# Optimization experiments

Hardware: AMD Instinct MI355X
Metric: run time of the kernel (lower is better)

The kernel has to match this reference:

```python
import jax, jax.numpy as jnp
import numpy as np

# pywt db4 analysis filters (dec_lo, dec_hi), length 8
DEC_LO = np.array([-0.010597401784997278, 0.032883011666982945, 0.030841381835986965,
                   -0.18703481171888114, -0.02798376941698385, 0.6308807679295904,
                   0.7148465705525415, 0.23037781330885523], dtype=np.float32)
DEC_HI = np.array([-0.23037781330885523, 0.7148465705525415, -0.6308807679295904,
                   -0.02798376941698385, 0.18703481171888114, 0.030841381835986965,
                   -0.032883011666982945, -0.010597401784997278], dtype=np.float32)


def setup_inputs() -> dict:
    key = jax.random.key(0)
    x = jax.random.normal(key, (32, 3, 512, 512), dtype=jnp.float32)
    dec = jnp.stack([jnp.asarray(DEC_LO), jnp.asarray(DEC_HI)])  # (2, 8)
    return {"x": x, "dec": dec}


def _afb1d_last(x, dec):
    """Analysis filter bank along last axis: circular pad (end), stride-2
    cross-correlation with lo/hi filters. x: (..., L) -> (lo, hi) each (..., L//2)."""
    L = x.shape[-1]
    taps = dec.shape[-1]
    pad = taps - 1
    xp = jnp.concatenate([x, x[..., :pad]], axis=-1)          # circular pad at end
    flat = xp.reshape(-1, 1, xp.shape[-1])                    # (N, 1, L+pad)
    out = jax.lax.conv_general_dilated(
        flat, dec[:, None, :], window_strides=(2,), padding='VALID',
        dimension_numbers=('NCH', 'OIH', 'NCH'))              # (N, 2, L//2)
    out = out.reshape(*x.shape[:-1], 2, L // 2)
    return out[..., 0, :], out[..., 1, :]


def reference(x, dec):
    B, C, H, W = x.shape
    xr = x.reshape(B * C, H, W)
    # row pass (along W)
    lo_w, hi_w = _afb1d_last(xr, dec)                         # (BC, H, W//2)
    # column pass (along H): move H to last axis
    lo_t = jnp.swapaxes(lo_w, -2, -1)                         # (BC, W//2, H)
    hi_t = jnp.swapaxes(hi_w, -2, -1)
    ll, lh = _afb1d_last(lo_t, dec)                           # (BC, W//2, H//2)
    hl, hh = _afb1d_last(hi_t, dec)
    coeffs = jnp.stack([ll, lh, hl, hh], axis=1)              # (BC, 4, W//2, H//2)
    coeffs = jnp.swapaxes(coeffs, -2, -1)                     # (BC, 4, H//2, W//2)
    return coeffs.reshape(B, C * 4, H // 2, W // 2)
```

## Files before the change

kernel.cpp:

```cpp
#include <hip/hip_runtime.h>


#define TI 8
#define TJ 64
#define PR (2*TI + 6)
#define PC 136
#define NG ((PR * PC) / 4)
#define HH 512
#define WW 512

typedef float v2f __attribute__((ext_vector_type(2)));
typedef const __attribute__((address_space(1))) void gas_t;
typedef __attribute__((address_space(3))) void las_t;

__global__ __launch_bounds__(256)
void dwt2d_db4_kernel(const float* __restrict__ x,
                      const float* __restrict__ dec,
                      float* __restrict__ out) {
    __shared__ __align__(16) float sm_x[PR * PC];
    __shared__ __align__(16) float sm_lo[PR][TJ];
    __shared__ __align__(16) float sm_hi[PR][TJ];

    const int tid  = threadIdx.x;
    const int wid  = tid >> 6;
    const int jt   = blockIdx.x;
    const int it   = blockIdx.y;
    const int bc   = blockIdx.z;

    const int rowBase = it * (2 * TI);
    const int colBase = jt * (2 * TJ);

    float flo[8], fhi[8];
#pragma unroll
    for (int k = 0; k < 8; ++k) { flo[k] = dec[k]; fhi[k] = dec[8 + k]; }

    const float* xb = x + (size_t)bc * HH * WW;

#pragma unroll
    for (int k = 0; k < 3; ++k) {
        int g = k * 256 + tid;
        las_t* lp = (las_t*)((char*)sm_x + k * 4096 + wid * 1024);
        if (g < NG) {
            int r  = g / 34;
            int c4 = g - r * 34;
            int gr = rowBase + r;  if (gr >= HH) gr -= HH;
            int gc = colBase + 4 * c4; if (gc >= WW) gc -= WW;
            const float* gp = xb + gr * WW + gc;
            __builtin_amdgcn_global_load_lds((gas_t*)gp, lp, 16, 0, 0);
        }
    }
    __syncthreads();

    for (int task = tid; task < PR * (TJ / 2); task += 256) {
        int r = task >> 5;
        int t = task & 31;
        const float* xr = &sm_x[r * PC + 4 * t];
        float4 v0 = *(const float4*)(xr);
        float4 v1 = *(const float4*)(xr + 4);
        float4 v2 = *(const float4*)(xr + 8);
        float w[12] = { v0.x, v0.y, v0.z, v0.w,
                        v1.x, v1.y, v1.z, v1.w,
                        v2.x, v2.y, v2.z, v2.w };
        float lo0 = 0.f, hi0 = 0.f, lo1 = 0.f, hi1 = 0.f;
#pragma unroll
        for (int q = 0; q < 8; ++q) {
            lo0 += w[q]     * flo[q];
            hi0 += w[q]     * fhi[q];
            lo1 += w[q + 2] * flo[q];
            hi1 += w[q + 2] * fhi[q];
        }
        *(float2*)&sm_lo[r][2 * t] = make_float2(lo0, lo1);
        *(float2*)&sm_hi[r][2 * t] = make_float2(hi0, hi1);
    }
    __syncthreads();

    {
        int i  = tid >> 5;
        int j0 = (tid & 31) * 2;
        float ll0=0.f, ll1=0.f, lh0=0.f, lh1=0.f;
        float hl0=0.f, hl1=0.f, hh0=0.f, hh1=0.f;
#pragma unroll
        for (int p = 0; p < 8; ++p) {
            float2 a = *(const float2*)&sm_lo[2 * i + p][j0];
            float2 b = *(const float2*)&sm_hi[2 * i + p][j0];
            float cl = flo[p], ch = fhi[p];
            ll0 += a.x * cl; ll1 += a.y * cl;
            lh0 += a.x * ch; lh1 += a.y * ch;
            hl0 += b.x * cl; hl1 += b.y * cl;
            hh0 += b.x * ch; hh1 += b.y * ch;
        }
        int oi = it * TI + i;
        int oj = jt * TJ + j0;
        size_t base = ((size_t)(bc * 4) * 256 + oi) * 256 + oj;
        v2f ll = { ll0, ll1 }, lh = { lh0, lh1 };
        v2f hl = { hl0, hl1 }, hh = { hh0, hh1 };
        __builtin_nontemporal_store(ll, (v2f*)&out[base]);
        __builtin_nontemporal_store(lh, (v2f*)&out[base + 1 * 65536]);
        __builtin_nontemporal_store(hl, (v2f*)&out[base + 2 * 65536]);
        __builtin_nontemporal_store(hh, (v2f*)&out[base + 3 * 65536]);
    }
}

extern "C" void kernel_launch(void* const* d_in, const int* in_sizes, int n_in,
                              void* d_out, int out_size, void* d_ws, size_t ws_size,
                              hipStream_t stream) {
    const float* x   = (const float*)d_in[0];
    const float* dec = (const float*)d_in[1];
    float* out = (float*)d_out;

    dim3 grid(256 / TJ, 256 / TI, 96);
    dim3 block(256);
    dwt2d_db4_kernel<<<grid, block, 0, stream>>>(x, dec, out);
}
```

Measured before the change: 172.6 us.

## Make kernel persistent with double-buffered async LDS tile prefetch

Replaces the one-tile-per-block grid with 1024 persistent blocks, each processing 12 consecutive tiles. The next tile is staged into a second LDS buffer with global_load_lds while the current one is filtered, and waits use explicit vmcnt/lgkmcnt barriers. The aim is to hide global load latency and cut launch/setup overhead per tile. The cost is doubled input LDS, which may lower occupancy, and fragile hand-tuned wait counts, where vmcnt(4) must match the number of outstanding stores and loads.

```diff
diff --git a/kernel.cpp b/kernel.cpp
--- a/kernel.cpp
+++ b/kernel.cpp
@@ -8,96 +8,127 @@
 #define NG ((PR * PC) / 4)
 #define HH 512
 #define WW 512
+#define NTILES 12288
+#define GRID 1024
+#define TPB (NTILES / GRID)
 
 typedef float v2f __attribute__((ext_vector_type(2)));
 typedef const __attribute__((address_space(1))) void gas_t;
 typedef __attribute__((address_space(3))) void las_t;
 
-__global__ __launch_bounds__(256)
+__device__ __forceinline__ void stage_tile(const float* __restrict__ x, int tile,
+                                           char* lds_base, int tid, int wid) {
+    const int jt = tile & 3;
+    const int it = (tile >> 2) & 31;
+    const int bc = tile >> 7;
+    const float* xb = x + (size_t)bc * (HH * WW);
+    const int rowBase = it * (2 * TI);
+    const int colBase = jt * (2 * TJ);
+#pragma unroll
+    for (int k = 0; k < 3; ++k) {
+        int g = k * 256 + tid;
+        las_t* lp = (las_t*)(lds_base + k * 4096 + wid * 1024);
+        if (g < NG) {
+            int r  = g / 34;
+            int c4 = g - r * 34;
+            int gr = rowBase + r;      if (gr >= HH) gr -= HH;
+            int gc = colBase + 4 * c4; if (gc >= WW) gc -= WW;
+            __builtin_amdgcn_global_load_lds((gas_t*)(xb + gr * WW + gc), lp, 16, 0, 0);
+        }
+    }
+}
+
+__global__ __launch_bounds__(256, 4)
 void dwt2d_db4_kernel(const float* __restrict__ x,
                       const float* __restrict__ dec,
                       float* __restrict__ out) {
-    __shared__ __align__(16) float sm_x[PR * PC];
+    __shared__ __align__(16) float sm_x[2][PR * PC];
     __shared__ __align__(16) float sm_lo[PR][TJ];
     __shared__ __align__(16) float sm_hi[PR][TJ];
 
-    const int tid  = threadIdx.x;
-    const int wid  = tid >> 6;
-    const int jt   = blockIdx.x;
-    const int it   = blockIdx.y;
-    const int bc   = blockIdx.z;
-
-    const int rowBase = it * (2 * TI);
-    const int colBase = jt * (2 * TJ);
+    const int tid = threadIdx.x;
+    const int wid = tid >> 6;
 
     float flo[8], fhi[8];
 #pragma unroll
     for (int k = 0; k < 8; ++k) { flo[k] = dec[k]; fhi[k] = dec[8 + k]; }
 
-    const float* xb = x + (size_t)bc * HH * WW;
+    const int bid   = blockIdx.x;
+    const int chunk = (bid & 7) * (GRID / 8) + (bid >> 3);
+    const int t0    = chunk * TPB;
 
+    stage_tile(x, t0, (char*)sm_x[0], tid, wid);
+    asm volatile("s_waitcnt vmcnt(0)" ::: "memory");
+    __builtin_amdgcn_sched_barrier(0);
+    __builtin_amdgcn_s_barrier();
+
+    for (int k = 0; k < TPB; ++k) {
+        const int tile = t0 + k;
+        const int jt = tile & 3;
+        const int it = (tile >> 2) & 31;
+        const int bc = tile >> 7;
+        const float* bx = sm_x[k & 1];
+
+        if (k + 1 < TPB)
+            stage_tile(x, tile + 1, (char*)sm_x[(k + 1) & 1], tid, wid);
+
+        for (int task = tid; task < PR * (TJ / 2); task += 256) {
+            int r = task >> 5;
+            int t = task & 31;
+            const float* xr = &bx[r * PC + 4 * t];
+            float4 v0 = *(const float4*)(xr);
+            float4 v1 = *(const float4*)(xr + 4);
+            float4 v2 = *(const float4*)(xr + 8);
+            float w[12] = { v0.x, v0.y, v0.z, v0.w,
+                            v1.x, v1.y, v1.z, v1.w,
+                            v2.x, v2.y, v2.z, v2.w };
+            float lo0 = 0.f, hi0 = 0.f, lo1 = 0.f, hi1 = 0.f;
 #pragma unroll
-    for (int k = 0; k < 3; ++k) {
-        int g = k * 256 + tid;
-        las_t* lp = (las_t*)((char*)sm_x + k * 4096 + wid * 1024);
-        if (g < NG) {
-            int r  = g / 34;
-            int c4 = g - r * 34;
-            int gr = rowBase + r;  if (gr >= HH) gr -= HH;
-            int gc = colBase + 4 * c4; if (gc >= WW) gc -= WW;
-            const float* gp = xb + gr * WW + gc;
-            __builtin_amdgcn_global_load_lds((gas_t*)gp, lp, 16, 0, 0);
+            for (int q = 0; q < 8; ++q) {
+                lo0 += w[q]     * flo[q];
+                hi0 += w[q]     * fhi[q];
+                lo1 += w[q + 2] * flo[q];
+                hi1 += w[q + 2] * fhi[q];
+            }
+            *(float2*)&sm_lo[r][2 * t] = make_float2(lo0, lo1);
+            *(float2*)&sm_hi[r][2 * t] = make_float2(hi0, hi1);
         }
-    }
-    __syncthreads();
 
-    for (int task = tid; task < PR * (TJ / 2); task += 256) {
-        int r = task >> 5;
-        int t = task & 31;
-        const float* xr = &sm_x[r * PC + 4 * t];
-        float4 v0 = *(const float4*)(xr);
-        float4 v1 = *(const float4*)(xr + 4);
-        float4 v2 = *(const float4*)(xr + 8);
-        float w[12] = { v0.x, v0.y, v0.z, v0.w,
-                        v1.x, v1.y, v1.z, v1.w,
-                        v2.x, v2.y, v2.z, v2.w };
-        float lo0 = 0.f, hi0 = 0.f, lo1 = 0.f, hi1 = 0.f;
+        asm volatile("s_waitcnt lgkmcnt(0)" ::: "memory");
+        __builtin_amdgcn_sched_barrier(0);
+        __builtin_amdgcn_s_barrier();
+
+        {
+            int i  = tid >> 5;
+            int j0 = (tid & 31) * 2;
+            float ll0=0.f, ll1=0.f, lh0=0.f, lh1=0.f;
+            float hl0=0.f, hl1=0.f, hh0=0.f, hh1=0.f;
 #pragma unroll
-        for (int q = 0; q < 8; ++q) {
-            lo0 += w[q]     * flo[q];
-            hi0 += w[q]     * fhi[q];
-            lo1 += w[q + 2] * flo[q];
-            hi1 += w[q + 2] * fhi[q];
+            for (int p = 0; p < 8; ++p) {
+                float2 a = *(const float2*)&sm_lo[2 * i + p][j0];
+                float2 b = *(const float2*)&sm_hi[2 * i + p][j0];
+                float cl = flo[p], ch = fhi[p];
+                ll0 += a.x * cl; ll1 += a.y * cl;
+                lh0 += a.x * ch; lh1 += a.y * ch;
+                hl0 += b.x * cl; hl1 += b.y * cl;
+                hh0 += b.x * ch; hh1 += b.y * ch;
+            }
+            int oi = it * TI + i;
+            int oj = jt * TJ + j0;
+            size_t base = ((size_t)(bc * 4) * 256 + oi) * 256 + oj;
+            v2f ll = { ll0, ll1 }, lh = { lh0, lh1 };
+            v2f hl = { hl0, hl1 }, hh = { hh0, hh1 };
+            __builtin_nontemporal_store(ll, (v2f*)&out[base]);
+            __builtin_nontemporal_store(lh, (v2f*)&out[base + 1 * 65536]);
+            __builtin_nontemporal_store(hl, (v2f*)&out[base + 2 * 65536]);
+            __builtin_nontemporal_store(hh, (v2f*)&out[base + 3 * 65536]);
         }
-        *(float2*)&sm_lo[r][2 * t] = make_float2(lo0, lo1);
-        *(float2*)&sm_hi[r][2 * t] = make_float2(hi0, hi1);
-    }
-    __syncthreads();
 
-    {
-        int i  = tid >> 5;
-        int j0 = (tid & 31) * 2;
-        float ll0=0.f, ll1=0.f, lh0=0.f, lh1=0.f;
-        float hl0=0.f, hl1=0.f, hh0=0.f, hh1=0.f;
-#pragma unroll
-        for (int p = 0; p < 8; ++p) {
-            float2 a = *(const float2*)&sm_lo[2 * i + p][j0];
-            float2 b = *(const float2*)&sm_hi[2 * i + p][j0];
-            float cl = flo[p], ch = fhi[p];
-            ll0 += a.x * cl; ll1 += a.y * cl;
-            lh0 += a.x * ch; lh1 += a.y * ch;
-            hl0 += b.x * cl; hl1 += b.y * cl;
-            hh0 += b.x * ch; hh1 += b.y * ch;
+        if (k + 1 < TPB) {
+            asm volatile("s_waitcnt vmcnt(4)" ::: "memory");
+            __builtin_amdgcn_sched_barrier(0);
+            __builtin_amdgcn_s_barrier();
         }
-        int oi = it * TI + i;
-        int oj = jt * TJ + j0;
-        size_t base = ((size_t)(bc * 4) * 256 + oi) * 256 + oj;
-        v2f ll = { ll0, ll1 }, lh = { lh0, lh1 };
-        v2f hl = { hl0, hl1 }, hh = { hh0, hh1 };
-        __builtin_nontemporal_store(ll, (v2f*)&out[base]);
-        __builtin_nontemporal_store(lh, (v2f*)&out[base + 1 * 65536]);
-        __builtin_nontemporal_store(hl, (v2f*)&out[base + 2 * 65536]);
-        __builtin_nontemporal_store(hh, (v2f*)&out[base + 3 * 65536]);
     }
 }
 
@@ -108,7 +139,7 @@
     const float* dec = (const float*)d_in[1];
     float* out = (float*)d_out;
 
-    dim3 grid(256 / TJ, 256 / TI, 96);
+    dim3 grid(GRID);
     dim3 block(256);
     dwt2d_db4_kernel<<<grid, block, 0, stream>>>(x, dec, out);
 }
```

New measurement: 185.4 us. +7.4%, slower.

## Halve row tile height and swizzle flattened block index across XCDs

Applied to the files above, without the earlier changes.

Reduces the tile from 8 to 4 output rows per block, so each block loads a smaller 14-row halo tile and each thread produces one output column instead of two. The grid becomes a flattened 1D index remapped so that consecutive blocks, which round-robin across XCDs, land on different row tiles. That mapping is meant to improve L2 locality for the overlapping halo rows. The cost is higher halo redundancy (14 rows loaded per 8 input rows instead of 22 per 16) and twice as many blocks.

```diff
diff --git a/kernel.cpp b/kernel.cpp
--- a/kernel.cpp
+++ b/kernel.cpp
@@ -1,7 +1,7 @@
 #include <hip/hip_runtime.h>
 
 
-#define TI 8
+#define TI 4
 #define TJ 64
 #define PR (2*TI + 6)
 #define PC 136
@@ -9,7 +9,6 @@
 #define HH 512
 #define WW 512
 
-typedef float v2f __attribute__((ext_vector_type(2)));
 typedef const __attribute__((address_space(1))) void gas_t;
 typedef __attribute__((address_space(3))) void las_t;
 
@@ -21,11 +20,14 @@
     __shared__ __align__(16) float sm_lo[PR][TJ];
     __shared__ __align__(16) float sm_hi[PR][TJ];
 
-    const int tid  = threadIdx.x;
-    const int wid  = tid >> 6;
-    const int jt   = blockIdx.x;
-    const int it   = blockIdx.y;
-    const int bc   = blockIdx.z;
+    const int tid = threadIdx.x;
+    const int wid = tid >> 6;
+
+    const int n  = blockIdx.x;
+    const int m  = n >> 3;
+    const int jt = m & 3;
+    const int it = (n & 7) * 8 + ((m >> 2) & 7);
+    const int bc = m >> 5;
 
     const int rowBase = it * (2 * TI);
     const int colBase = jt * (2 * TJ);
@@ -37,7 +39,7 @@
     const float* xb = x + (size_t)bc * HH * WW;
 
 #pragma unroll
-    for (int k = 0; k < 3; ++k) {
+    for (int k = 0; k < 2; ++k) {
         int g = k * 256 + tid;
         las_t* lp = (las_t*)((char*)sm_x + k * 4096 + wid * 1024);
         if (g < NG) {
@@ -75,29 +77,24 @@
     __syncthreads();
 
     {
-        int i  = tid >> 5;
-        int j0 = (tid & 31) * 2;
-        float ll0=0.f, ll1=0.f, lh0=0.f, lh1=0.f;
-        float hl0=0.f, hl1=0.f, hh0=0.f, hh1=0.f;
+        int i = tid >> 6;
+        int j = tid & 63;
+        float ll = 0.f, lh = 0.f, hl = 0.f, hh = 0.f;
 #pragma unroll
         for (int p = 0; p < 8; ++p) {
-            float2 a = *(const float2*)&sm_lo[2 * i + p][j0];
-            float2 b = *(const float2*)&sm_hi[2 * i + p][j0];
+            float a = sm_lo[2 * i + p][j];
+            float b = sm_hi[2 * i + p][j];
             float cl = flo[p], ch = fhi[p];
-            ll0 += a.x * cl; ll1 += a.y * cl;
-            lh0 += a.x * ch; lh1 += a.y * ch;
-            hl0 += b.x * cl; hl1 += b.y * cl;
-            hh0 += b.x * ch; hh1 += b.y * ch;
+            ll += a * cl; lh += a * ch;
+            hl += b * cl; hh += b * ch;
         }
         int oi = it * TI + i;
-        int oj = jt * TJ + j0;
+        int oj = jt * TJ + j;
         size_t base = ((size_t)(bc * 4) * 256 + oi) * 256 + oj;
-        v2f ll = { ll0, ll1 }, lh = { lh0, lh1 };
-        v2f hl = { hl0, hl1 }, hh = { hh0, hh1 };
-        __builtin_nontemporal_store(ll, (v2f*)&out[base]);
-        __builtin_nontemporal_store(lh, (v2f*)&out[base + 1 * 65536]);
-        __builtin_nontemporal_store(hl, (v2f*)&out[base + 2 * 65536]);
-        __builtin_nontemporal_store(hh, (v2f*)&out[base + 3 * 65536]);
+        __builtin_nontemporal_store(ll, &out[base]);
+        __builtin_nontemporal_store(lh, &out[base + 1 * 65536]);
+        __builtin_nontemporal_store(hl, &out[base + 2 * 65536]);
+        __builtin_nontemporal_store(hh, &out[base + 3 * 65536]);
     }
 }
 
@@ -108,7 +105,7 @@
     const float* dec = (const float*)d_in[1];
     float* out = (float*)d_out;
 
-    dim3 grid(256 / TJ, 256 / TI, 96);
+    dim3 grid(4 * 64 * 96);
     dim3 block(256);
     dwt2d_db4_kernel<<<grid, block, 0, stream>>>(x, dec, out);
 }
```

After: 172.0 us. About the same (-0.3%).
